# Kernel tuning notes

Measured on AMD Instinct MI355X. Metric: run time of the kernel, lower is better.

Reference implementation:

```python
import jax, jax.numpy as jnp
import numpy as np

D_MODEL = 1024
D_FF = 4096
N_HEADS = 16
D_HEAD = D_MODEL // N_HEADS
BSZ, SEQ = 2, 2048
EPS = 1e-6


def layer_norm(x, lam, beta):
    # torch impl: (x - mu) / (std_biased + eps) * lambda + beta
    mu = jnp.mean(x, axis=-1, keepdims=True)
    sigma = jnp.sqrt(jnp.mean((x - mu) ** 2, axis=-1, keepdims=True)) + EPS
    return (x - mu) / sigma * lam + beta


def setup_inputs() -> dict:
    key = jax.random.key(0)
    ks = jax.random.split(key, 10)
    s = 0.02
    x = jax.random.normal(ks[0], (BSZ, SEQ, D_MODEL), dtype=jnp.float32)
    mask = jnp.ones((BSZ, 1, 1, SEQ), dtype=jnp.int32)
    # nn.Linear weights stored [out, in]; y = x @ W.T
    Wq = jax.random.normal(ks[1], (D_MODEL, D_MODEL), dtype=jnp.float32) * s
    Wk = jax.random.normal(ks[2], (D_MODEL, D_MODEL), dtype=jnp.float32) * s
    Wv = jax.random.normal(ks[3], (D_MODEL, D_MODEL), dtype=jnp.float32) * s
    Wo = jax.random.normal(ks[4], (D_MODEL, D_MODEL), dtype=jnp.float32) * s
    w1 = jax.random.normal(ks[5], (D_FF, D_MODEL), dtype=jnp.float32) * s
    b1 = jnp.zeros((D_FF,), dtype=jnp.float32)
    w2 = jax.random.normal(ks[6], (D_MODEL, D_FF), dtype=jnp.float32) * s
    b2 = jnp.zeros((D_MODEL,), dtype=jnp.float32)
    g1 = jnp.ones((D_MODEL,), dtype=jnp.float32)
    be1 = jnp.zeros((D_MODEL,), dtype=jnp.float32)
    g2 = jnp.ones((D_MODEL,), dtype=jnp.float32)
    be2 = jnp.zeros((D_MODEL,), dtype=jnp.float32)
    return {"x": x, "mask": mask, "Wq": Wq, "Wk": Wk, "Wv": Wv, "Wo": Wo,
            "w1": w1, "b1": b1, "w2": w2, "b2": b2,
            "g1": g1, "be1": be1, "g2": g2, "be2": be2}


def reference(x, mask, Wq, Wk, Wv, Wo, w1, b1, w2, b2, g1, be1, g2, be2):
    b, s, _ = x.shape
    # projections (y = x @ W.T), split heads -> [b, h, s, dh]
    def split_heads(t):
        return t.reshape(b, s, N_HEADS, D_HEAD).transpose(0, 2, 1, 3)
    Q = split_heads(x @ Wq.T)
    K = split_heads(x @ Wk.T)
    V = split_heads(x @ Wv.T)
    score = jnp.einsum('bhqd,bhkd->bhqk', Q, K) / jnp.sqrt(jnp.float32(D_HEAD))
    score = jnp.where(mask == 0, -jnp.inf, score)
    attn = jax.nn.softmax(score, axis=-1)
    out = jnp.einsum('bhqk,bhkd->bhqd', attn, V)
    out = out.transpose(0, 2, 1, 3).reshape(b, s, D_MODEL)
    x1 = out @ Wo.T
    x2 = layer_norm(x1 + x, g1, be1)
    x3 = jax.nn.relu(x2 @ w1.T + b1) @ w2.T + b2
    x4 = layer_norm(x2 + x3, g2, be2)
    return x4
```

## Files before the change

### kernel.cpp

```cpp
#include <hip/hip_runtime.h>
#include <math.h>

typedef __attribute__((ext_vector_type(8))) short bf16x8;
typedef __attribute__((ext_vector_type(4))) float f32x4;
typedef __attribute__((ext_vector_type(8))) unsigned short us8;
typedef unsigned short u16;
typedef unsigned int u32;

constexpr int BSZ = 2, SEQ = 2048, DM = 1024, DFF = 4096, NH = 16, DH = 64;
constexpr int MROWS = BSZ * SEQ;

__device__ __forceinline__ float bf2f(u16 u) {
  union { unsigned int i; float f; } v; v.i = ((unsigned int)u) << 16; return v.f;
}
__device__ __forceinline__ u16 f2bf(float f) {
  union { float f; unsigned int i; } v; v.f = f;
  unsigned int r = v.i + 0x7fffu + ((v.i >> 16) & 1u);
  return (u16)(r >> 16);
}

#define GLOAD16(gp, lp) __builtin_amdgcn_global_load_lds( \
    (const __attribute__((address_space(1))) void*)(gp),  \
    (__attribute__((address_space(3))) void*)(lp), 16, 0, 0)
#define GLOAD4(gp, lp) __builtin_amdgcn_global_load_lds( \
    (const __attribute__((address_space(1))) void*)(gp),  \
    (__attribute__((address_space(3))) void*)(lp), 4, 0, 0)

__global__ __launch_bounds__(256) void cvt_all(
    const float* __restrict__ x, const float* __restrict__ Wq,
    const float* __restrict__ Wk, const float* __restrict__ Wv,
    const float* __restrict__ Wo, const float* __restrict__ w1,
    const float* __restrict__ w2, u16* __restrict__ xb,
    u16* __restrict__ Wqkvb, u16* __restrict__ Wob,
    u16* __restrict__ w1b, u16* __restrict__ w2b) {
  constexpr int M1 = 1 << 20;
  const int i = (blockIdx.x * 256 + threadIdx.x) * 8;
  const float* src;
  u16* dst;
  int off;
  if (i < 4 * M1)        { src = x;  dst = xb;            off = i;           }
  else if (i < 5 * M1)   { src = Wq; dst = Wqkvb;         off = i - 4 * M1;  }
  else if (i < 6 * M1)   { src = Wk; dst = Wqkvb + M1;    off = i - 5 * M1;  }
  else if (i < 7 * M1)   { src = Wv; dst = Wqkvb + 2 * M1; off = i - 6 * M1; }
  else if (i < 8 * M1)   { src = Wo; dst = Wob;           off = i - 7 * M1;  }
  else if (i < 12 * M1)  { src = w1; dst = w1b;           off = i - 8 * M1;  }
  else                   { src = w2; dst = w2b;           off = i - 12 * M1; }
  const float4 a = *(const float4*)(src + off);
  const float4 b = *(const float4*)(src + off + 4);
  uint4 o;
  o.x = f2bf(a.x) | ((unsigned)f2bf(a.y) << 16);
  o.y = f2bf(a.z) | ((unsigned)f2bf(a.w) << 16);
  o.z = f2bf(b.x) | ((unsigned)f2bf(b.y) << 16);
  o.w = f2bf(b.z) | ((unsigned)f2bf(b.w) << 16);
  *(uint4*)(dst + off) = o;
}

template <int BM, int BN, bool BIAS, bool RELU, bool OBF16>
__global__ __launch_bounds__(256) void gemm_bf16(
    const u16* __restrict__ A, const u16* __restrict__ B,
    const float* __restrict__ bias, float* __restrict__ Cf,
    u16* __restrict__ Cb, int M, int N, int K) {
  constexpr int MI = BM / 32, NI = BN / 32;
  __shared__ u16 As[2][BM * 32];
  __shared__ u16 Bs[2][BN * 32];
  const int tid = threadIdx.x;
  const int lane = tid & 63, wid = tid >> 6;

  const int nwg = gridDim.x * gridDim.y;
  int id = blockIdx.y * gridDim.x + blockIdx.x;
  id = (id & 7) * (nwg >> 3) + (id >> 3);
  const int bx = id % gridDim.x, by = id / gridDim.x;

  const int row0 = by * BM, col0 = bx * BN;
  const int wr = (wid >> 1) * (BM / 2), wc = (wid & 1) * (BN / 2);
  const int fr = lane & 15, hi = lane >> 4;

  f32x4 acc[MI][NI];
#pragma unroll
  for (int i = 0; i < MI; ++i)
#pragma unroll
    for (int j = 0; j < NI; ++j) acc[i][j] = {0.f, 0.f, 0.f, 0.f};

  const int sr = tid >> 2;
  const int se = (tid & 3) * 8;

#define STAGE(buf, k0)                                                        \
  {                                                                           \
    _Pragma("unroll")                                                         \
    for (int c = 0; c < BM * 64; c += 4096) {                                 \
      const int r = (c >> 6) + sr;                                            \
      GLOAD16(A + (size_t)(row0 + r) * K + ((k0) + se),                       \
              ((char*)As[buf]) + c + tid * 16);                               \
    }                                                                         \
    _Pragma("unroll")                                                         \
    for (int c = 0; c < BN * 64; c += 4096) {                                 \
      const int r = (c >> 6) + sr;                                            \
      GLOAD16(B + (size_t)(col0 + r) * K + ((k0) + se),                       \
              ((char*)Bs[buf]) + c + tid * 16);                               \
    }                                                                         \
  }

  STAGE(0, 0);
  __syncthreads();

  const int NIT = K / 32;
  for (int it = 0; it < NIT; ++it) {
    const int cur = it & 1;
    if (it + 1 < NIT) STAGE(cur ^ 1, (it + 1) * 32);

    bf16x8 af[MI], bv[NI];
#pragma unroll
    for (int mi = 0; mi < MI; ++mi)
      af[mi] = *(const bf16x8*)&As[cur][(wr + mi * 16 + fr) * 32 + hi * 8];
#pragma unroll
    for (int ni = 0; ni < NI; ++ni)
      bv[ni] = *(const bf16x8*)&Bs[cur][(wc + ni * 16 + fr) * 32 + hi * 8];
#pragma unroll
    for (int mi = 0; mi < MI; ++mi)
#pragma unroll
      for (int ni = 0; ni < NI; ++ni)
        acc[mi][ni] = __builtin_amdgcn_mfma_f32_16x16x32_bf16(
            af[mi], bv[ni], acc[mi][ni], 0, 0, 0);
    __syncthreads();
  }
#undef STAGE

  const int erow = row0 + wr + (hi << 2);
  const int ecol0 = col0 + wc;
#pragma unroll
  for (int ni = 0; ni < NI; ++ni) {
    const int col = ecol0 + ni * 16 + fr;
    const float bvv = BIAS ? bias[col] : 0.f;
#pragma unroll
    for (int mi = 0; mi < MI; ++mi) {
      const int rbase = erow + mi * 16;
#pragma unroll
      for (int j = 0; j < 4; ++j) {
        float v = acc[mi][ni][j] + bvv;
        if (RELU) v = fmaxf(v, 0.f);
        const size_t idx = (size_t)(rbase + j) * N + col;
        if (OBF16) Cb[idx] = f2bf(v); else Cf[idx] = v;
      }
    }
  }
}

__global__ __launch_bounds__(512) void attn_mfma(
    const u16* __restrict__ QKV, const int* __restrict__ mask,
    u16* __restrict__ Ob) {
  constexpr int KB = 64, QB = 128, NT = SEQ / KB;
  __shared__ u16 Kl[2][KB * 64];
  __shared__ u16 Vt[2][64 * KB];
  __shared__ int ml[2][KB];

  const int tid = threadIdx.x;
  const int lane = tid & 63, wid = tid >> 6;
  const int q0 = blockIdx.x * QB;
  const int bh = blockIdx.y;
  const int b = bh >> 4, h = bh & 15;
  const size_t base = (size_t)b * SEQ * 3072;
  const int fr = lane & 15, g = lane >> 4;

  const u16* qp = QKV + base + (size_t)(q0 + wid * 16 + fr) * 3072 + h * 64 + g * 8;
  bf16x8 qf0, qf1;
  {
    const float QSC = 0.18033688f;
    const us8 ua = *(const us8*)qp;
    const us8 ub = *(const us8*)(qp + 32);
    u32 pa[4], pb[4];
#pragma unroll
    for (int i = 0; i < 4; ++i) {
      const float a0 = bf2f(ua[2 * i]) * QSC, a1 = bf2f(ua[2 * i + 1]) * QSC;
      const float b0 = bf2f(ub[2 * i]) * QSC, b1 = bf2f(ub[2 * i + 1]) * QSC;
      asm("v_cvt_pk_bf16_f32 %0, %1, %2" : "=v"(pa[i]) : "v"(a0), "v"(a1));
      asm("v_cvt_pk_bf16_f32 %0, %1, %2" : "=v"(pb[i]) : "v"(b0), "v"(b1));
    }
    union { u32 d[4]; bf16x8 v; } c0, c1;
#pragma unroll
    for (int i = 0; i < 4; ++i) { c0.d[i] = pa[i]; c1.d[i] = pb[i]; }
    qf0 = c0.v; qf1 = c1.v;
  }

  const int krow = wid * 8 + (lane >> 3);
  const int kcol = 8 * ((lane & 7) ^ (lane >> 3));
  const u16* ksrc = QKV + base + 1024 + h * 64 + kcol;
  const int kdst = wid * 1024 + lane * 16;

  const int va = (tid & 255) >> 3;
  const int vq = tid & 7;
  const u16* vsrc = QKV + base + 2048 + h * 64 + vq * 8;
  const bool vstage = (wid < 4);

  f32x4 o[4] = {{0.f,0.f,0.f,0.f},{0.f,0.f,0.f,0.f},{0.f,0.f,0.f,0.f},{0.f,0.f,0.f,0.f}};
  float mreg = -3e38f, lreg = 0.f;

  {
    GLOAD16(ksrc + (size_t)krow * 3072, (char*)Kl[0] + kdst);
    if (wid == 4) GLOAD4(mask + b * SEQ + lane, (char*)ml[0] + lane * 4);
    if (vstage) {
      const us8 v0 = *(const us8*)(vsrc + (size_t)(2 * va) * 3072);
      const us8 v1 = *(const us8*)(vsrc + (size_t)(2 * va + 1) * 3072);
      char* vb = (char*)Vt[0];
#pragma unroll
      for (int i = 0; i < 8; ++i) {
        const int d = vq * 8 + i;
        const u32 wv = (u32)(u16)v0[i] | ((u32)(u16)v1[i] << 16);
        *(u32*)(vb + d * 128 + ((4 * va) ^ ((vq ^ i) << 4))) = wv;
      }
    }
  }
  __syncthreads();

  for (int it = 0; it < NT; ++it) {
    const int cur = it & 1, nxt = cur ^ 1;
    const int ktn = (it + 1) * KB;
    const bool pre = (it + 1 < NT);
    us8 v0 = {}, v1 = {};
    if (pre) {
      GLOAD16(ksrc + (size_t)(ktn + krow) * 3072, (char*)Kl[nxt] + kdst);
      if (wid == 4) GLOAD4(mask + b * SEQ + ktn + lane, (char*)ml[nxt] + lane * 4);
      if (vstage) {
        v0 = *(const us8*)(vsrc + (size_t)(ktn + 2 * va) * 3072);
        v1 = *(const us8*)(vsrc + (size_t)(ktn + 2 * va + 1) * 3072);
      }
    }

    f32x4 s[4];
#pragma unroll
    for (int t16 = 0; t16 < 4; ++t16) {
      const int kr = t16 * 16 + fr;
      const char* krp = (const char*)Kl[cur] + kr * 128;
      const int sw = (kr & 7) << 4;
      const bf16x8 kf0 = *(const bf16x8*)(krp + ((g * 16) ^ sw));
      const bf16x8 kf1 = *(const bf16x8*)(krp + ((g * 16 + 64) ^ sw));
      f32x4 a = {0.f, 0.f, 0.f, 0.f};
      a = __builtin_amdgcn_mfma_f32_16x16x32_bf16(kf0, qf0, a, 0, 0, 0);
      a = __builtin_amdgcn_mfma_f32_16x16x32_bf16(kf1, qf1, a, 0, 0, 0);
      s[t16] = a;
    }

#pragma unroll
    for (int t16 = 0; t16 < 4; ++t16) {
      const int4 mv = *(const int4*)&ml[cur][t16 * 16 + g * 4];
      const int* mp = (const int*)&mv;
#pragma unroll
      for (int j = 0; j < 4; ++j)
        if (mp[j] == 0) s[t16][j] = -3e38f;
    }

    float rmax = s[0][0];
#pragma unroll
    for (int t16 = 0; t16 < 4; ++t16)
#pragma unroll
      for (int j = 0; j < 4; ++j) rmax = fmaxf(rmax, s[t16][j]);

    if (!__all(rmax <= mreg + 12.f)) {
      rmax = fmaxf(rmax, __shfl_xor(rmax, 16));
      rmax = fmaxf(rmax, __shfl_xor(rmax, 32));
      const float mn = fmaxf(mreg, rmax);
      float sc;
      asm("v_exp_f32 %0, %1" : "=v"(sc) : "v"(mreg - mn));
      mreg = mn;
      lreg *= sc;
#pragma unroll
      for (int j = 0; j < 4; ++j) {
        const float scj = __shfl(sc, (g << 4) + g * 4 + j);
#pragma unroll
        for (int dt = 0; dt < 4; ++dt) o[dt][j] *= scj;
      }
    }

    float p[4][4];
#pragma unroll
    for (int t16 = 0; t16 < 4; ++t16)
#pragma unroll
      for (int j = 0; j < 4; ++j) {
        float e;
        asm("v_exp_f32 %0, %1" : "=v"(e) : "v"(s[t16][j] - mreg));
        p[t16][j] = e;
        lreg += e;
      }

    u32 plo[4], phi[4];
#pragma unroll
    for (int t16 = 0; t16 < 4; ++t16) {
      asm("v_cvt_pk_bf16_f32 %0, %1, %2"
          : "=v"(plo[t16]) : "v"(p[t16][0]), "v"(p[t16][1]));
      asm("v_cvt_pk_bf16_f32 %0, %1, %2"
          : "=v"(phi[t16]) : "v"(p[t16][2]), "v"(p[t16][3]));
    }

#pragma unroll
    for (int kh = 0; kh < 2; ++kh) {
      u32 fd[4];
#pragma unroll
      for (int hf = 0; hf < 2; ++hf) {
        const int sl = fr + ((((g & 1) << 1) + hf) << 4);
        const u32 c0l = (u32)__shfl((int)plo[kh * 2], sl);
        const u32 c0h = (u32)__shfl((int)phi[kh * 2], sl);
        const u32 c1l = (u32)__shfl((int)plo[kh * 2 + 1], sl);
        const u32 c1h = (u32)__shfl((int)phi[kh * 2 + 1], sl);
        const bool s1 = ((g >> 1) & 1) != 0;
        fd[hf * 2] = s1 ? c1l : c0l;
        fd[hf * 2 + 1] = s1 ? c1h : c0h;
      }
      union { u32 d[4]; bf16x8 v; } uu;
      uu.d[0] = fd[0]; uu.d[1] = fd[1]; uu.d[2] = fd[2]; uu.d[3] = fd[3];
      const bf16x8 pf = uu.v;
#pragma unroll
      for (int dt = 0; dt < 4; ++dt) {
        const int d = dt * 16 + fr;
        const int xd = (((d >> 3) ^ d) & 7) << 4;
        const bf16x8 vf = *(const bf16x8*)((const char*)Vt[cur] + d * 128 +
                                           ((g * 16 + kh * 64) ^ xd));
        o[dt] = __builtin_amdgcn_mfma_f32_16x16x32_bf16(pf, vf, o[dt], 0, 0, 0);
      }
    }

    if (pre && vstage) {
      char* vb = (char*)Vt[nxt];
#pragma unroll
      for (int i = 0; i < 8; ++i) {
        const int d = vq * 8 + i;
        const u32 wv = (u32)(u16)v0[i] | ((u32)(u16)v1[i] << 16);
        *(u32*)(vb + d * 128 + ((4 * va) ^ ((vq ^ i) << 4))) = wv;
      }
    }
    __syncthreads();
  }

  lreg += __shfl_xor(lreg, 16);
  lreg += __shfl_xor(lreg, 32);
  const float inv = 1.f / lreg;
#pragma unroll
  for (int j = 0; j < 4; ++j) {
    const float invj = __shfl(inv, (g << 4) + g * 4 + j);
    const int qrow = q0 + wid * 16 + g * 4 + j;
    u16* orow = Ob + (size_t)(b * SEQ + qrow) * DM + h * 64;
#pragma unroll
    for (int dt = 0; dt < 4; ++dt)
      orow[dt * 16 + fr] = f2bf(o[dt][j] * invj);
  }
}

template <bool ABF, bool BBF, bool OBF>
__global__ __launch_bounds__(256) void ln_add(const void* __restrict__ Ap,
                                              const void* __restrict__ Bp,
                                              const float* __restrict__ g,
                                              const float* __restrict__ be,
                                              void* __restrict__ outp) {
  __shared__ float red[2][4];
  __shared__ float mu_s, sig_s;
  const int row = blockIdx.x;
  const int tid = threadIdx.x;

  float4 a, b;
  if (ABF) {
    const ushort4 u = *(const ushort4*)((const u16*)Ap + (size_t)row * DM + tid * 4);
    a = make_float4(bf2f(u.x), bf2f(u.y), bf2f(u.z), bf2f(u.w));
  } else {
    a = *(const float4*)((const float*)Ap + (size_t)row * DM + tid * 4);
  }
  if (BBF) {
    const ushort4 u = *(const ushort4*)((const u16*)Bp + (size_t)row * DM + tid * 4);
    b = make_float4(bf2f(u.x), bf2f(u.y), bf2f(u.z), bf2f(u.w));
  } else {
    b = *(const float4*)((const float*)Bp + (size_t)row * DM + tid * 4);
  }
  float4 s = make_float4(a.x + b.x, a.y + b.y, a.z + b.z, a.w + b.w);

  float sum = s.x + s.y + s.z + s.w;
  float sq = s.x * s.x + s.y * s.y + s.z * s.z + s.w * s.w;
#pragma unroll
  for (int off = 32; off >= 1; off >>= 1) {
    sum += __shfl_xor(sum, off);
    sq += __shfl_xor(sq, off);
  }
  const int wid = tid >> 6;
  if ((tid & 63) == 0) { red[0][wid] = sum; red[1][wid] = sq; }
  __syncthreads();
  if (tid == 0) {
    float ts = red[0][0] + red[0][1] + red[0][2] + red[0][3];
    float tq = red[1][0] + red[1][1] + red[1][2] + red[1][3];
    float mu = ts * (1.f / DM);
    float var = tq * (1.f / DM) - mu * mu;
    mu_s = mu;
    sig_s = sqrtf(fmaxf(var, 0.f)) + 1e-6f;
  }
  __syncthreads();
  const float mu = mu_s, inv = 1.f / sig_s;
  const float4 gv = *(const float4*)(g + tid * 4);
  const float4 bv = *(const float4*)(be + tid * 4);
  float4 o;
  o.x = (s.x - mu) * inv * gv.x + bv.x;
  o.y = (s.y - mu) * inv * gv.y + bv.y;
  o.z = (s.z - mu) * inv * gv.z + bv.z;
  o.w = (s.w - mu) * inv * gv.w + bv.w;
  if (OBF) {
    u16* op = (u16*)outp + (size_t)row * DM + tid * 4;
    ushort4 o4;
    o4.x = f2bf(o.x); o4.y = f2bf(o.y); o4.z = f2bf(o.z); o4.w = f2bf(o.w);
    *(ushort4*)op = o4;
  } else {
    *(float4*)((float*)outp + (size_t)row * DM + tid * 4) = o;
  }
}

extern "C" void kernel_launch(void* const* d_in, const int* in_sizes, int n_in,
                              void* d_out, int out_size, void* d_ws,
                              size_t ws_size, hipStream_t stream) {
  const float* x  = (const float*)d_in[0];
  const int* mask = (const int*)d_in[1];
  const float* Wq = (const float*)d_in[2];
  const float* Wk = (const float*)d_in[3];
  const float* Wv = (const float*)d_in[4];
  const float* Wo = (const float*)d_in[5];
  const float* w1 = (const float*)d_in[6];
  const float* b1 = (const float*)d_in[7];
  const float* w2 = (const float*)d_in[8];
  const float* b2 = (const float*)d_in[9];
  const float* g1 = (const float*)d_in[10];
  const float* be1 = (const float*)d_in[11];
  const float* g2 = (const float*)d_in[12];
  const float* be2 = (const float*)d_in[13];
  float* out = (float*)d_out;
  float* ws = (float*)d_ws;

  u16*   QKVb  = (u16*)(ws + 0);
  u16*   xb    = (u16*)(ws + 6291456);
  u16*   Wqkvb = (u16*)(ws + 8388608);
  u16*   Wob   = (u16*)(ws + 9961472);
  u16*   w1b   = (u16*)(ws + 10485760);
  u16*   w2b   = (u16*)(ws + 12582912);
  u16*   Obf   = (u16*)(ws + 14680064);
  u16*   X1b   = (u16*)(ws + 16777216);
  u16*   X2b   = (u16*)(ws + 20971520);
  u16*   X3b   = (u16*)(ws + 23068672);
  u16*   Hb    = (u16*)(ws + 0);

  const dim3 blk(256);

  cvt_all<<<8192, blk, 0, stream>>>(x, Wq, Wk, Wv, Wo, w1, w2,
                                    xb, Wqkvb, Wob, w1b, w2b);

  gemm_bf16<128, 128, false, false, true><<<dim3(3072 / 128, MROWS / 128), blk, 0, stream>>>(
      xb, Wqkvb, nullptr, nullptr, QKVb, MROWS, 3072, DM);

  attn_mfma<<<dim3(SEQ / 128, BSZ * NH), dim3(512), 0, stream>>>(QKVb, mask, Obf);

  gemm_bf16<64, 128, false, false, true><<<dim3(DM / 128, MROWS / 64), blk, 0, stream>>>(
      Obf, Wob, nullptr, nullptr, X1b, MROWS, DM, DM);

  ln_add<true, false, true><<<dim3(MROWS), blk, 0, stream>>>(X1b, x, g1, be1, X2b);

  gemm_bf16<128, 128, true, true, true><<<dim3(DFF / 128, MROWS / 128), blk, 0, stream>>>(
      X2b, w1b, b1, nullptr, Hb, MROWS, DFF, DM);

  gemm_bf16<64, 128, true, false, true><<<dim3(DM / 128, MROWS / 64), blk, 0, stream>>>(
      Hb, w2b, b2, nullptr, X3b, MROWS, DM, DFF);

  ln_add<true, true, false><<<dim3(MROWS), blk, 0, stream>>>(X2b, X3b, g2, be2, out);
}
```

Baseline: 271.6 us.

## Add 256x256 tile 8-wave GEMM kernel for QKV and FFN1 projections

Adds a new bf16 MFMA GEMM with 256x256 output tiles, 512 threads, a K-step of 64, XOR-swizzled LDS staging through global_load_lds, and a phased MFMA schedule with setprio and barriers. The QKV projection and the first FFN GEMM now use it instead of the 128x128 kernel. The larger tile raises arithmetic intensity and cuts global traffic per FLOP. The grid becomes much smaller (12x16 and 16x16 workgroups), which may underfill the 256 CUs, and the kernel needs 128 KB of LDS and heavy register use.

```diff
diff --git a/kernel.cpp b/kernel.cpp
--- a/kernel.cpp
+++ b/kernel.cpp
@@ -55,6 +55,148 @@
   *(uint4*)(dst + off) = o;
 }
 
+template <bool BIAS, bool RELU>
+__global__ __launch_bounds__(512, 2) void gemm256(
+    const u16* __restrict__ A, const u16* __restrict__ B,
+    const float* __restrict__ bias, u16* __restrict__ Cb,
+    int M, int N, int K) {
+  __shared__ u16 As[2][256 * 64];
+  __shared__ u16 Bs[2][256 * 64];
+  const int tid = threadIdx.x;
+  const int lane = tid & 63, wid = tid >> 6;
+
+  const int nwg = gridDim.x * gridDim.y;
+  int id = blockIdx.y * gridDim.x + blockIdx.x;
+  id = (id & 7) * (nwg >> 3) + (id >> 3);
+  const int bx = id % gridDim.x, by = id / gridDim.x;
+
+  const int row0 = by * 256, col0 = bx * 256;
+  const int wm = wid >> 2, wn = wid & 3;
+  const int fr = lane & 15, hi = lane >> 4;
+
+  f32x4 acc[8][4];
+#pragma unroll
+  for (int i = 0; i < 8; ++i)
+#pragma unroll
+    for (int j = 0; j < 4; ++j) acc[i][j] = {0.f, 0.f, 0.f, 0.f};
+
+  const int tr = tid >> 3, tp = tid & 7;
+
+#define STAGE8(buf, k0)                                                       \
+  {                                                                           \
+    _Pragma("unroll")                                                         \
+    for (int l = 0; l < 4; ++l) {                                             \
+      const int r = l * 64 + tr;                                              \
+      GLOAD16(A + (size_t)(row0 + r) * K + (k0) + ((tp ^ (r & 7)) * 8),       \
+              ((char*)As[buf]) + l * 8192 + tid * 16);                        \
+    }                                                                         \
+    _Pragma("unroll")                                                         \
+    for (int l = 0; l < 4; ++l) {                                             \
+      const int r = l * 64 + tr;                                              \
+      GLOAD16(B + (size_t)(col0 + r) * K + (k0) + ((tp ^ (r & 7)) * 8),       \
+              ((char*)Bs[buf]) + l * 8192 + tid * 16);                        \
+    }                                                                         \
+  }
+
+#define AFRAG(buf, mi, kh)                                                    \
+  (*(const bf16x8*)&As[buf][(wm * 128 + (mi) * 16 + fr) * 64 +                \
+      ((((kh) * 4 + hi) ^ ((wm * 128 + (mi) * 16 + fr) & 7)) * 8)])
+#define BFRAG(buf, ni, kh)                                                    \
+  (*(const bf16x8*)&Bs[buf][(wn * 64 + (ni) * 16 + fr) * 64 +                 \
+      ((((kh) * 4 + hi) ^ ((wn * 64 + (ni) * 16 + fr) & 7)) * 8)])
+
+  STAGE8(0, 0);
+  __syncthreads();
+
+  const int NT = K / 64;
+  for (int t = 0; t < NT; ++t) {
+    const int cur = t & 1, nxt = cur ^ 1;
+    bf16x8 afr[4], bfr[4];
+
+    if (t + 1 < NT) STAGE8(nxt, (t + 1) * 64);
+#pragma unroll
+    for (int m = 0; m < 4; ++m) afr[m] = AFRAG(cur, m, 0);
+#pragma unroll
+    for (int n = 0; n < 4; ++n) bfr[n] = BFRAG(cur, n, 0);
+    asm volatile("s_waitcnt lgkmcnt(0)" ::: "memory");
+    __builtin_amdgcn_sched_barrier(0);
+    __builtin_amdgcn_s_setprio(1);
+#pragma unroll
+    for (int m = 0; m < 4; ++m)
+#pragma unroll
+      for (int n = 0; n < 4; ++n)
+        acc[m][n] = __builtin_amdgcn_mfma_f32_16x16x32_bf16(
+            afr[m], bfr[n], acc[m][n], 0, 0, 0);
+    __builtin_amdgcn_s_setprio(0);
+    __builtin_amdgcn_s_barrier();
+
+#pragma unroll
+    for (int m = 0; m < 4; ++m) afr[m] = AFRAG(cur, 4 + m, 0);
+    asm volatile("s_waitcnt lgkmcnt(0)" ::: "memory");
+    __builtin_amdgcn_sched_barrier(0);
+    __builtin_amdgcn_s_setprio(1);
+#pragma unroll
+    for (int m = 0; m < 4; ++m)
+#pragma unroll
+      for (int n = 0; n < 4; ++n)
+        acc[4 + m][n] = __builtin_amdgcn_mfma_f32_16x16x32_bf16(
+            afr[m], bfr[n], acc[4 + m][n], 0, 0, 0);
+    __builtin_amdgcn_s_setprio(0);
+    __builtin_amdgcn_s_barrier();
+
+#pragma unroll
+    for (int m = 0; m < 4; ++m) afr[m] = AFRAG(cur, m, 1);
+#pragma unroll
+    for (int n = 0; n < 4; ++n) bfr[n] = BFRAG(cur, n, 1);
+    asm volatile("s_waitcnt lgkmcnt(0)" ::: "memory");
+    __builtin_amdgcn_sched_barrier(0);
+    __builtin_amdgcn_s_setprio(1);
+#pragma unroll
+    for (int m = 0; m < 4; ++m)
+#pragma unroll
+      for (int n = 0; n < 4; ++n)
+        acc[m][n] = __builtin_amdgcn_mfma_f32_16x16x32_bf16(
+            afr[m], bfr[n], acc[m][n], 0, 0, 0);
+    __builtin_amdgcn_s_setprio(0);
+    __builtin_amdgcn_s_barrier();
+
+#pragma unroll
+    for (int m = 0; m < 4; ++m) afr[m] = AFRAG(cur, 4 + m, 1);
+    asm volatile("s_waitcnt lgkmcnt(0)" ::: "memory");
+    __builtin_amdgcn_sched_barrier(0);
+    __builtin_amdgcn_s_setprio(1);
+#pragma unroll
+    for (int m = 0; m < 4; ++m)
+#pragma unroll
+      for (int n = 0; n < 4; ++n)
+        acc[4 + m][n] = __builtin_amdgcn_mfma_f32_16x16x32_bf16(
+            afr[m], bfr[n], acc[4 + m][n], 0, 0, 0);
+    __builtin_amdgcn_s_setprio(0);
+    asm volatile("s_waitcnt vmcnt(0)" ::: "memory");
+    __builtin_amdgcn_s_barrier();
+    __builtin_amdgcn_sched_barrier(0);
+  }
+#undef STAGE8
+#undef AFRAG
+#undef BFRAG
+
+  const int erow0 = row0 + wm * 128 + hi * 4;
+#pragma unroll
+  for (int n = 0; n < 4; ++n) {
+    const int col = col0 + wn * 64 + n * 16 + fr;
+    const float bvv = BIAS ? bias[col] : 0.f;
+#pragma unroll
+    for (int m = 0; m < 8; ++m) {
+#pragma unroll
+      for (int j = 0; j < 4; ++j) {
+        float v = acc[m][n][j] + bvv;
+        if (RELU) v = fmaxf(v, 0.f);
+        Cb[(size_t)(erow0 + m * 16 + j) * N + col] = f2bf(v);
+      }
+    }
+  }
+}
+
 template <int BM, int BN, bool BIAS, bool RELU, bool OBF16>
 __global__ __launch_bounds__(256) void gemm_bf16(
     const u16* __restrict__ A, const u16* __restrict__ B,
@@ -443,8 +585,8 @@
   cvt_all<<<8192, blk, 0, stream>>>(x, Wq, Wk, Wv, Wo, w1, w2,
                                     xb, Wqkvb, Wob, w1b, w2b);
 
-  gemm_bf16<128, 128, false, false, true><<<dim3(3072 / 128, MROWS / 128), blk, 0, stream>>>(
-      xb, Wqkvb, nullptr, nullptr, QKVb, MROWS, 3072, DM);
+  gemm256<false, false><<<dim3(3072 / 256, MROWS / 256), dim3(512), 0, stream>>>(
+      xb, Wqkvb, nullptr, QKVb, MROWS, 3072, DM);
 
   attn_mfma<<<dim3(SEQ / 128, BSZ * NH), dim3(512), 0, stream>>>(QKVb, mask, Obf);
 
@@ -453,8 +595,8 @@
 
   ln_add<true, false, true><<<dim3(MROWS), blk, 0, stream>>>(X1b, x, g1, be1, X2b);
 
-  gemm_bf16<128, 128, true, true, true><<<dim3(DFF / 128, MROWS / 128), blk, 0, stream>>>(
-      X2b, w1b, b1, nullptr, Hb, MROWS, DFF, DM);
+  gemm256<true, true><<<dim3(DFF / 256, MROWS / 256), dim3(512), 0, stream>>>(
+      X2b, w1b, b1, Hb, MROWS, DFF, DM);
 
   gemm_bf16<64, 128, true, false, true><<<dim3(DM / 128, MROWS / 64), blk, 0, stream>>>(
       Hb, w2b, b2, nullptr, X3b, MROWS, DM, DFF);
```

Result: no change. 273.8 us (+0.8%).
